# Kernel optimization log

Measured on AMD Instinct MI355X. Metric: run time of the kernel, lower is better.

Reference implementation:

```python
import jax, jax.numpy as jnp
import numpy as np

D_MODEL, EXPAND, D_STATE, D_CONV, HEADDIM = 1024, 2, 64, 4, 64
D_INNER = EXPAND * D_MODEL          # 2048
NHEADS = D_INNER // HEADDIM         # 32
CONV_DIM = D_INNER + 2 * D_STATE    # x, B, C go through the depthwise conv
D_IN_PROJ = 2 * D_INNER + 2 * D_STATE + NHEADS  # z, xBC, dt
EPS = 1e-5


def setup_inputs() -> dict:
    key = jax.random.key(0)
    ks = jax.random.split(key, 16)
    s = 0.02
    inp = {
        "x": jax.random.normal(ks[0], (2, 2048, D_MODEL), jnp.float32),
        "ln1_w": jnp.ones((D_MODEL,), jnp.float32),
        "ln1_b": jnp.zeros((D_MODEL,), jnp.float32),
        "in_proj_w": jax.random.normal(ks[1], (D_IN_PROJ, D_MODEL), jnp.float32) * s,
        "conv_w": jax.random.normal(ks[2], (CONV_DIM, D_CONV), jnp.float32) * 0.3,
        "conv_b": jnp.zeros((CONV_DIM,), jnp.float32),
        # dt_bias so that softplus(dt+dt_bias) lands in ~[1e-3, 0.1] (mamba2 init)
        "dt_bias": jnp.log(jnp.expm1(jnp.exp(jax.random.uniform(ks[3], (NHEADS,), jnp.float32, jnp.log(1e-3), jnp.log(0.1))))),
        "A_log": jnp.log(jax.random.uniform(ks[4], (NHEADS,), jnp.float32, 1.0, 16.0)),
        "D": jnp.ones((NHEADS,), jnp.float32),
        "norm_w": jnp.ones((D_INNER,), jnp.float32),
        "out_proj_w": jax.random.normal(ks[5], (D_MODEL, D_INNER), jnp.float32) * s,
        "ln2_w": jnp.ones((D_MODEL,), jnp.float32),
        "ln2_b": jnp.zeros((D_MODEL,), jnp.float32),
        "mlp_w1": jax.random.normal(ks[6], (4 * D_MODEL, D_MODEL), jnp.float32) * s,
        "mlp_b1": jnp.zeros((4 * D_MODEL,), jnp.float32),
        "mlp_w2": jax.random.normal(ks[7], (D_MODEL, 4 * D_MODEL), jnp.float32) * s,
        "mlp_b2": jnp.zeros((D_MODEL,), jnp.float32),
    }
    return inp


def _layernorm(x, w, b):
    mu = jnp.mean(x, axis=-1, keepdims=True)
    var = jnp.mean(jnp.square(x - mu), axis=-1, keepdims=True)
    return (x - mu) * jax.lax.rsqrt(var + EPS) * w + b


def _mamba2(x, in_proj_w, conv_w, conv_b, dt_bias, A_log, D, norm_w, out_proj_w):
    Bt, L, _ = x.shape
    zxbcdt = x @ in_proj_w.T                                  # [B,L,D_IN_PROJ]
    z = zxbcdt[..., :D_INNER]
    xBC = zxbcdt[..., D_INNER:D_INNER + CONV_DIM]
    dt = jax.nn.softplus(zxbcdt[..., D_INNER + CONV_DIM:] + dt_bias)  # [B,L,H]
    # causal depthwise conv1d, kernel D_CONV, then SiLU
    xp = jnp.pad(xBC, ((0, 0), (D_CONV - 1, 0), (0, 0)))
    conv = conv_b
    for k in range(D_CONV):
        conv = conv + xp[:, k:k + L, :] * conv_w[:, k]
    xBC = jax.nn.silu(conv)
    xs = xBC[..., :D_INNER].reshape(Bt, L, NHEADS, HEADDIM)   # [B,L,H,P]
    Bm = xBC[..., D_INNER:D_INNER + D_STATE]                  # [B,L,N] (ngroups=1)
    Cm = xBC[..., D_INNER + D_STATE:]                         # [B,L,N]
    A = -jnp.exp(A_log)                                       # [H]

    def step(h, inp):
        x_t, dt_t, B_t, C_t = inp                             # [B,H,P],[B,H],[B,N],[B,N]
        dA = jnp.exp(dt_t * A)                                # [B,H]
        h = h * dA[:, :, None, None] + (dt_t[:, :, None] * x_t)[..., None] * B_t[:, None, None, :]
        y = jnp.einsum('bhpn,bn->bhp', h, C_t)
        return h, y

    h0 = jnp.zeros((Bt, NHEADS, HEADDIM, D_STATE), x.dtype)
    xsT = jnp.moveaxis(xs, 1, 0)
    dtT = jnp.moveaxis(dt, 1, 0)
    BT = jnp.moveaxis(Bm, 1, 0)
    CT = jnp.moveaxis(Cm, 1, 0)
    _, ys = jax.lax.scan(step, h0, (xsT, dtT, BT, CT))        # ys: [L,B,H,P]
    y = jnp.moveaxis(ys, 0, 1) + xs * D[None, None, :, None]  # skip D
    y = y.reshape(Bt, L, D_INNER)
    # gated RMSNorm: rmsnorm(y * silu(z)) * norm_w
    y = y * jax.nn.silu(z)
    y = y * jax.lax.rsqrt(jnp.mean(jnp.square(y), axis=-1, keepdims=True) + EPS) * norm_w
    return y @ out_proj_w.T


def reference(x, ln1_w, ln1_b, in_proj_w, conv_w, conv_b, dt_bias, A_log, D,
              norm_w, out_proj_w, ln2_w, ln2_b, mlp_w1, mlp_b1, mlp_w2, mlp_b2):
    res = x
    h = _layernorm(x, ln1_w, ln1_b)
    h = _mamba2(h, in_proj_w, conv_w, conv_b, dt_bias, A_log, D, norm_w, out_proj_w)
    x = res + h
    res = x
    h = _layernorm(x, ln2_w, ln2_b)
    h = jax.nn.gelu(h @ mlp_w1.T + mlp_b1, approximate=False) @ mlp_w2.T + mlp_b2
    return res + h
```

## Files before the change

kernel.cpp:

```cpp
#include <hip/hip_runtime.h>
#include <hip/hip_bf16.h>
#include <math.h>

using bf16 = __hip_bfloat16;
typedef __attribute__((ext_vector_type(8))) short short8;
typedef __attribute__((ext_vector_type(4))) float floatx4;

#define SEQLEN   2048
#define ROWS     4096
#define DMODEL   1024
#define DINNER   2048
#define NHEADS   32
#define HEADDIM  64
#define DSTATE   64
#define CONVDIM  2176
#define DINPROJ  4256
#define NCHUNK   32

__device__ __forceinline__ float b2f(bf16 x) { return __bfloat162float(x); }
__device__ __forceinline__ bf16  f2b(float x) { return __float2bfloat16(x); }
__device__ __forceinline__ float s2f(short s) { union { short s; bf16 b; } u; u.s = s; return b2f(u.b); }
__device__ __forceinline__ short f2s(float f) { union { short s; bf16 b; } u; u.b = f2b(f); return u.s; }
__device__ __forceinline__ float tof(float x) { return x; }
__device__ __forceinline__ float tof(bf16 x)  { return __bfloat162float(x); }

typedef __attribute__((address_space(1))) void v_as1;
typedef __attribute__((address_space(3))) void v_as3;
__device__ __forceinline__ void gload_lds16(const void* g, void* l) {
  __builtin_amdgcn_global_load_lds((v_as1*)(g), (v_as3*)(l), 16, 0, 0);
}

__global__ void cvt_kernel(const float* __restrict__ in, bf16* __restrict__ out, int n4) {
  int i = blockIdx.x * 256 + threadIdx.x;
  if (i < n4) {
    float4 v = ((const float4*)in)[i];
    union { bf16 h[4]; uint2 u; } r;
    r.h[0] = f2b(v.x); r.h[1] = f2b(v.y); r.h[2] = f2b(v.z); r.h[3] = f2b(v.w);
    ((uint2*)out)[i] = r.u;
  }
}

__device__ __forceinline__ void block_reduce_2(float& a, float& b) {
#pragma unroll
  for (int off = 32; off > 0; off >>= 1) {
    a += __shfl_xor(a, off);
    b += __shfl_xor(b, off);
  }
  __shared__ float ra[4], rb[4];
  int w = threadIdx.x >> 6;
  if ((threadIdx.x & 63) == 0) { ra[w] = a; rb[w] = b; }
  __syncthreads();
  a = ra[0] + ra[1] + ra[2] + ra[3];
  b = rb[0] + rb[1] + rb[2] + rb[3];
}

template<typename TIN>
__global__ void ln_kernel(const TIN* __restrict__ x, const float* __restrict__ w,
                          const float* __restrict__ b, bf16* __restrict__ out)
{
  int row = blockIdx.x;
  int tid = threadIdx.x;
  float v[4]; float s = 0.f, sq = 0.f;
#pragma unroll
  for (int k = 0; k < 4; ++k) {
    int c = k * 256 + tid;
    float xv = tof(x[(size_t)row * DMODEL + c]);
    v[k] = xv; s += xv; sq += xv * xv;
  }
  block_reduce_2(s, sq);
  float mu  = s * (1.f / DMODEL);
  float var = sq * (1.f / DMODEL) - mu * mu;
  float rs  = rsqrtf(var + 1e-5f);
#pragma unroll
  for (int k = 0; k < 4; ++k) {
    int c = k * 256 + tid;
    out[(size_t)row * DMODEL + c] = f2b((v[k] - mu) * rs * w[c] + b[c]);
  }
}

template<int EPI>
__device__ __forceinline__ void epi_store(float v, size_t off, int col,
                                          const float* bias, const void* resid, void* Cout)
{
  if (EPI == 0) {
    ((bf16*)Cout)[off] = f2b(v);
  } else if (EPI == 1) {
    v += bias[col];
    v = 0.5f * v * (1.f + erff(v * 0.70710678118654752f));
    ((bf16*)Cout)[off] = f2b(v);
  } else if (EPI == 2) {
    v += ((const float*)resid)[off];
    ((bf16*)Cout)[off] = f2b(v);
  } else {
    v += bias[col] + b2f(((const bf16*)resid)[off]);
    ((float*)Cout)[off] = v;
  }
}


template<int EPI>
__global__ __launch_bounds__(256, 2)
void gemm_bt(const bf16* __restrict__ A, const bf16* __restrict__ W,
             const float* __restrict__ bias, const void* __restrict__ resid,
             void* __restrict__ Cout, int M, int N, int K)
{
  __shared__ __align__(16) short Asl[128 * 64];
  __shared__ __align__(16) short Bsl[128 * 64];
  const int tid  = threadIdx.x;
  const int lane = tid & 63;
  const int wv   = tid >> 6;
  const int wm   = wv >> 1, wn = wv & 1;
  const int r16  = lane & 15, q = lane >> 4;
  const int m0   = blockIdx.x * 128;
  const int n0   = blockIdx.y * 128;

  floatx4 acc[4][4] = {};

  for (int k0 = 0; k0 < K; k0 += 64) {
#pragma unroll
    for (int it = 0; it < 4; ++it) {
      int idx = it * 256 + tid;
      int row = m0 + (idx >> 3);
      int cb  = (((idx & 7) ^ ((idx >> 3) & 7)) << 3);
      gload_lds16(A + (size_t)row * K + k0 + cb, &Asl[idx * 8]);
    }
#pragma unroll
    for (int it = 0; it < 4; ++it) {
      int idx = it * 256 + tid;
      int row = n0 + (idx >> 3);
      if (row > N - 1) row = N - 1;
      int cb  = (((idx & 7) ^ ((idx >> 3) & 7)) << 3);
      gload_lds16(W + (size_t)row * K + k0 + cb, &Bsl[idx * 8]);
    }
    __syncthreads();
#pragma unroll
    for (int kk = 0; kk < 64; kk += 32) {
      short8 af[4], bfr[4];
      const int lb = (kk >> 3) + q;
#pragma unroll
      for (int i = 0; i < 4; ++i) {
        int ar = wm * 64 + i * 16 + r16;
        af[i] = *(const short8*)&Asl[ar * 64 + ((lb ^ (ar & 7)) << 3)];
      }
#pragma unroll
      for (int j = 0; j < 4; ++j) {
        int br = wn * 64 + j * 16 + r16;
        bfr[j] = *(const short8*)&Bsl[br * 64 + ((lb ^ (br & 7)) << 3)];
      }
#pragma unroll
      for (int i = 0; i < 4; ++i)
#pragma unroll
        for (int j = 0; j < 4; ++j)
          acc[i][j] = __builtin_amdgcn_mfma_f32_16x16x32_bf16(af[i], bfr[j], acc[i][j], 0, 0, 0);
    }
    __syncthreads();
  }

#pragma unroll
  for (int i = 0; i < 4; ++i)
#pragma unroll
    for (int j = 0; j < 4; ++j)
#pragma unroll
      for (int r = 0; r < 4; ++r) {
        int row = m0 + wm * 64 + i * 16 + q * 4 + r;
        int col = n0 + wn * 64 + j * 16 + r16;
        if (col < N)
          epi_store<EPI>(acc[i][j][r], (size_t)row * N + col, col, bias, resid, Cout);
      }
}

template<int EPI>
__global__ __launch_bounds__(256, 4)
void gemm_bt_6464(const bf16* __restrict__ A, const bf16* __restrict__ W,
                  const float* __restrict__ bias, const void* __restrict__ resid,
                  void* __restrict__ Cout, int M, int N, int K)
{
  __shared__ __align__(16) short Asl[64 * 64];
  __shared__ __align__(16) short Bsl[64 * 64];
  const int tid  = threadIdx.x;
  const int lane = tid & 63;
  const int wv   = tid >> 6;
  const int wm   = wv >> 1, wn = wv & 1;
  const int r16  = lane & 15, q = lane >> 4;
  const int m0   = blockIdx.x * 64;
  const int n0   = blockIdx.y * 64;

  floatx4 acc[2][2] = {};

  for (int k0 = 0; k0 < K; k0 += 64) {
#pragma unroll
    for (int it = 0; it < 2; ++it) {
      int idx = it * 256 + tid;
      int cb  = (((idx & 7) ^ ((idx >> 3) & 7)) << 3);
      gload_lds16(A + (size_t)(m0 + (idx >> 3)) * K + k0 + cb, &Asl[idx * 8]);
    }
#pragma unroll
    for (int it = 0; it < 2; ++it) {
      int idx = it * 256 + tid;
      int cb  = (((idx & 7) ^ ((idx >> 3) & 7)) << 3);
      gload_lds16(W + (size_t)(n0 + (idx >> 3)) * K + k0 + cb, &Bsl[idx * 8]);
    }
    __syncthreads();
#pragma unroll
    for (int kk = 0; kk < 64; kk += 32) {
      short8 af[2], bfr[2];
      const int lb = (kk >> 3) + q;
#pragma unroll
      for (int i = 0; i < 2; ++i) {
        int ar = wm * 32 + i * 16 + r16;
        af[i] = *(const short8*)&Asl[ar * 64 + ((lb ^ (ar & 7)) << 3)];
      }
#pragma unroll
      for (int j = 0; j < 2; ++j) {
        int br = wn * 32 + j * 16 + r16;
        bfr[j] = *(const short8*)&Bsl[br * 64 + ((lb ^ (br & 7)) << 3)];
      }
#pragma unroll
      for (int i = 0; i < 2; ++i)
#pragma unroll
        for (int j = 0; j < 2; ++j)
          acc[i][j] = __builtin_amdgcn_mfma_f32_16x16x32_bf16(af[i], bfr[j], acc[i][j], 0, 0, 0);
    }
    __syncthreads();
  }

#pragma unroll
  for (int i = 0; i < 2; ++i)
#pragma unroll
    for (int j = 0; j < 2; ++j)
#pragma unroll
      for (int r = 0; r < 4; ++r) {
        int row = m0 + wm * 32 + i * 16 + q * 4 + r;
        int col = n0 + wn * 32 + j * 16 + r16;
        epi_store<EPI>(acc[i][j][r], (size_t)row * N + col, col, bias, resid, Cout);
      }
}

__global__ void conv_kernel(const bf16* __restrict__ zx, const float* __restrict__ cw,
                            const float* __restrict__ cb, const float* __restrict__ dtbias,
                            bf16* __restrict__ xbc, bf16* __restrict__ Bb,
                            bf16* __restrict__ Cbb, float* __restrict__ dtb)
{
  int row = blockIdx.x;
  int b = row >> 11, t = row & 2047;
  for (int c = threadIdx.x; c < CONVDIM; c += 256) {
    float acc = cb[c];
#pragma unroll
    for (int k = 0; k < 4; ++k) {
      int tt = t + k - 3;
      if (tt >= 0)
        acc += b2f(zx[((size_t)(b * SEQLEN + tt)) * DINPROJ + DINNER + c]) * cw[c * 4 + k];
    }
    float s = acc / (1.f + __expf(-acc));
    xbc[(size_t)row * CONVDIM + c] = f2b(s);
    if (c >= DINNER) {
      if (c < DINNER + DSTATE) Bb[row * DSTATE + (c - DINNER)] = f2b(s);
      else                     Cbb[row * DSTATE + (c - DINNER - DSTATE)] = f2b(s);
    }
  }
  if (threadIdx.x < NHEADS) {
    int hh = threadIdx.x;
    float raw = b2f(zx[(size_t)row * DINPROJ + DINNER + CONVDIM + hh]) + dtbias[hh];
    float dt = raw > 20.f ? raw : log1pf(__expf(raw));
    dtb[row * NHEADS + hh] = dt;
  }
}

__device__ __forceinline__ float wave_incl_prefix(float a, int lane) {
#pragma unroll
  for (int off = 1; off < 64; off <<= 1) {
    float o = __shfl_up(a, off);
    if (lane >= off) a += o;
  }
  return a;
}

__global__ __launch_bounds__(64)
void chunk_state_kernel(const bf16* __restrict__ xbc, const bf16* __restrict__ Bb,
                        const float* __restrict__ dtb, const float* __restrict__ A_log,
                        float* __restrict__ Sbuf, float* __restrict__ Pbuf)
{
  const int blk = blockIdx.x;
  const int c = blk & 31, h = (blk >> 5) & 31, b = blk >> 10;
  const int bh = b * 32 + h;
  const int lane = threadIdx.x;
  const int row = b * SEQLEN + c * 64 + lane;
  const float Ah = -__expf(A_log[h]);

  float dts = dtb[row * NHEADS + h];
  float E = wave_incl_prefix(dts * Ah, lane);
  float EQ = __shfl(E, 63);
  float w = __expf(EQ - E) * dts;
  if (lane == 63) Pbuf[bh * NCHUNK + c] = __expf(EQ);

  __shared__ __align__(16) short XwT[64 * 72];
  __shared__ __align__(16) short BT[64 * 72];

  const bf16* xrow = xbc + (size_t)row * CONVDIM + h * 64;
  const bf16* brow = Bb + (size_t)row * DSTATE;
#pragma unroll
  for (int i = 0; i < 8; ++i) {
    short8 xv = *(const short8*)(xrow + i * 8);
    short8 bv = *(const short8*)(brow + i * 8);
#pragma unroll
    for (int j = 0; j < 8; ++j) {
      XwT[(i * 8 + j) * 72 + lane] = f2s(w * s2f(xv[j]));
      BT[(i * 8 + j) * 72 + lane]  = bv[j];
    }
  }
  __syncthreads();

  const int r16 = lane & 15, q = lane >> 4;
  floatx4 acc[4][4] = {};
#pragma unroll
  for (int kk = 0; kk < 64; kk += 32) {
    short8 af[4], bfr[4];
#pragma unroll
    for (int i = 0; i < 4; ++i) af[i]  = *(const short8*)&XwT[(i * 16 + r16) * 72 + kk + q * 8];
#pragma unroll
    for (int j = 0; j < 4; ++j) bfr[j] = *(const short8*)&BT[(j * 16 + r16) * 72 + kk + q * 8];
#pragma unroll
    for (int i = 0; i < 4; ++i)
#pragma unroll
      for (int j = 0; j < 4; ++j)
        acc[i][j] = __builtin_amdgcn_mfma_f32_16x16x32_bf16(af[i], bfr[j], acc[i][j], 0, 0, 0);
  }
  float* Sout = Sbuf + (size_t)(bh * NCHUNK + c) * 4096;
#pragma unroll
  for (int i = 0; i < 4; ++i)
#pragma unroll
    for (int j = 0; j < 4; ++j)
#pragma unroll
      for (int r = 0; r < 4; ++r)
        Sout[(i * 16 + q * 4 + r) * 64 + (j * 16 + r16)] = acc[i][j][r];
}

__global__ __launch_bounds__(64)
void combine_kernel(const float* __restrict__ Sbuf, const float* __restrict__ Pbuf,
                    bf16* __restrict__ HinB)
{
  const int bh = blockIdx.x >> 2, slab = blockIdx.x & 3;
  const int base = slab * 1024 + threadIdx.x * 16;
  float h[16];
#pragma unroll
  for (int k = 0; k < 16; ++k) h[k] = 0.f;
  for (int c = 0; c < NCHUNK; ++c) {
    size_t off = (size_t)(bh * NCHUNK + c) * 4096 + base;
    union { short s[16]; uint4 q[2]; } pk;
#pragma unroll
    for (int k = 0; k < 16; ++k) pk.s[k] = f2s(h[k]);
    *(uint4*)(HinB + off)     = pk.q[0];
    *(uint4*)(HinB + off + 8) = pk.q[1];
    float P = Pbuf[bh * NCHUNK + c];
    const float4* S4 = (const float4*)(Sbuf + off);
#pragma unroll
    for (int k = 0; k < 4; ++k) {
      float4 s = S4[k];
      h[k*4+0] = h[k*4+0] * P + s.x;
      h[k*4+1] = h[k*4+1] * P + s.y;
      h[k*4+2] = h[k*4+2] * P + s.z;
      h[k*4+3] = h[k*4+3] * P + s.w;
    }
  }
}

__global__ __launch_bounds__(64)
void y_kernel(const bf16* __restrict__ xbc, const bf16* __restrict__ Bb,
              const bf16* __restrict__ Cbb, const float* __restrict__ dtb,
              const bf16* __restrict__ HinB, const float* __restrict__ A_log,
              const float* __restrict__ Dp, bf16* __restrict__ yout)
{
  const int blk = blockIdx.x;
  const int c = blk & 31, h = (blk >> 5) & 31, b = blk >> 10;
  const int bh = b * 32 + h;
  const int lane = threadIdx.x;
  const int row0 = b * SEQLEN + c * 64;
  const int row = row0 + lane;
  const float Ah = -__expf(A_log[h]);
  const float Dh = Dp[h];

  __shared__ __align__(16) short XdT[64 * 72];
  __shared__ __align__(16) short Msh[64 * 72];
  __shared__ float Esh[64];

  float dts = dtb[row * NHEADS + h];
  float E = wave_incl_prefix(dts * Ah, lane);
  Esh[lane] = E;

  const bf16* xrow = xbc + (size_t)row * CONVDIM + h * 64;
#pragma unroll
  for (int i = 0; i < 8; ++i) {
    short8 xv = *(const short8*)(xrow + i * 8);
#pragma unroll
    for (int j = 0; j < 8; ++j)
      XdT[(i * 8 + j) * 72 + lane] = f2s(dts * s2f(xv[j]));
  }
  __syncthreads();

  const int r16 = lane & 15, q = lane >> 4;

  floatx4 accg[4][4] = {};
#pragma unroll
  for (int kk = 0; kk < 64; kk += 32) {
    short8 af[4], bfr[4];
#pragma unroll
    for (int i = 0; i < 4; ++i)
      af[i]  = *(const short8*)(Cbb + (size_t)(row0 + i * 16 + r16) * DSTATE + kk + q * 8);
#pragma unroll
    for (int j = 0; j < 4; ++j)
      bfr[j] = *(const short8*)(Bb + (size_t)(row0 + j * 16 + r16) * DSTATE + kk + q * 8);
#pragma unroll
    for (int i = 0; i < 4; ++i)
#pragma unroll
      for (int j = 0; j < 4; ++j)
        accg[i][j] = __builtin_amdgcn_mfma_f32_16x16x32_bf16(af[i], bfr[j], accg[i][j], 0, 0, 0);
  }
#pragma unroll
  for (int i = 0; i < 4; ++i)
#pragma unroll
    for (int j = 0; j < 4; ++j)
#pragma unroll
      for (int r = 0; r < 4; ++r) {
        int t = i * 16 + q * 4 + r;
        int s = j * 16 + r16;
        float v = (s <= t) ? __expf(Esh[t] - Esh[s]) * accg[i][j][r] : 0.f;
        Msh[t * 72 + s] = f2s(v);
      }
  __syncthreads();

  floatx4 acc[4][4] = {};
#pragma unroll
  for (int kk = 0; kk < 64; kk += 32) {
    short8 af[4], bfr[4];
#pragma unroll
    for (int i = 0; i < 4; ++i) af[i]  = *(const short8*)&Msh[(i * 16 + r16) * 72 + kk + q * 8];
#pragma unroll
    for (int j = 0; j < 4; ++j) bfr[j] = *(const short8*)&XdT[(j * 16 + r16) * 72 + kk + q * 8];
#pragma unroll
    for (int i = 0; i < 4; ++i)
#pragma unroll
      for (int j = 0; j < 4; ++j)
        acc[i][j] = __builtin_amdgcn_mfma_f32_16x16x32_bf16(af[i], bfr[j], acc[i][j], 0, 0, 0);
  }
  float ei[4];
#pragma unroll
  for (int i = 0; i < 4; ++i) ei[i] = __expf(Esh[i * 16 + r16]);
  const bf16* hinp = HinB + (size_t)(bh * NCHUNK + c) * 4096;
#pragma unroll
  for (int kk = 0; kk < 64; kk += 32) {
    short8 af[4], bfr[4];
#pragma unroll
    for (int i = 0; i < 4; ++i) {
      short8 cv = *(const short8*)(Cbb + (size_t)(row0 + i * 16 + r16) * DSTATE + kk + q * 8);
#pragma unroll
      for (int jj = 0; jj < 8; ++jj) af[i][jj] = f2s(ei[i] * s2f(cv[jj]));
    }
#pragma unroll
    for (int j = 0; j < 4; ++j)
      bfr[j] = *(const short8*)(hinp + (j * 16 + r16) * 64 + kk + q * 8);
#pragma unroll
    for (int i = 0; i < 4; ++i)
#pragma unroll
      for (int j = 0; j < 4; ++j)
        acc[i][j] = __builtin_amdgcn_mfma_f32_16x16x32_bf16(af[i], bfr[j], acc[i][j], 0, 0, 0);
  }
#pragma unroll
  for (int i = 0; i < 4; ++i)
#pragma unroll
    for (int j = 0; j < 4; ++j)
#pragma unroll
      for (int r = 0; r < 4; ++r) {
        int t = i * 16 + q * 4 + r;
        int p = j * 16 + r16;
        int g = row0 + t;
        float y = acc[i][j][r] + Dh * b2f(xbc[(size_t)g * CONVDIM + h * 64 + p]);
        yout[(size_t)g * DINNER + h * 64 + p] = f2b(y);
      }
}

__global__ void gate_rms_kernel(const bf16* __restrict__ y, const bf16* __restrict__ zx,
                                const float* __restrict__ nw, bf16* __restrict__ yn)
{
  int row = blockIdx.x, tid = threadIdx.x;
  float v[8]; float ss = 0.f, dummy = 0.f;
#pragma unroll
  for (int k = 0; k < 8; ++k) {
    int c = k * 256 + tid;
    float z = b2f(zx[(size_t)row * DINPROJ + c]);
    float g = z / (1.f + __expf(-z));
    float val = b2f(y[(size_t)row * DINNER + c]) * g;
    v[k] = val; ss += val * val;
  }
  block_reduce_2(ss, dummy);
  float rs = rsqrtf(ss * (1.f / DINNER) + 1e-5f);
#pragma unroll
  for (int k = 0; k < 8; ++k) {
    int c = k * 256 + tid;
    yn[(size_t)row * DINNER + c] = f2b(v[k] * rs * nw[c]);
  }
}

extern "C" void kernel_launch(void* const* d_in, const int* in_sizes, int n_in,
                              void* d_out, int out_size, void* d_ws, size_t ws_size,
                              hipStream_t stream)
{
  const float* x         = (const float*)d_in[0];
  const float* ln1_w     = (const float*)d_in[1];
  const float* ln1_b     = (const float*)d_in[2];
  const float* in_proj_w = (const float*)d_in[3];
  const float* conv_w    = (const float*)d_in[4];
  const float* conv_b    = (const float*)d_in[5];
  const float* dt_bias   = (const float*)d_in[6];
  const float* A_log     = (const float*)d_in[7];
  const float* Dp        = (const float*)d_in[8];
  const float* norm_w    = (const float*)d_in[9];
  const float* out_proj_w= (const float*)d_in[10];
  const float* ln2_w     = (const float*)d_in[11];
  const float* ln2_b     = (const float*)d_in[12];
  const float* mlp_w1    = (const float*)d_in[13];
  const float* mlp_b1    = (const float*)d_in[14];
  const float* mlp_w2    = (const float*)d_in[15];
  const float* mlp_b2    = (const float*)d_in[16];

  char* ws = (char*)d_ws;
  bf16*  zx   = (bf16*)(ws + 0);
  bf16*  h1   = (bf16*)(ws + 34865152);
  bf16*  xbc  = (bf16*)(ws + 43253760);
  bf16*  Bb   = (bf16*)(ws + 61079552);
  bf16*  Cbb  = (bf16*)(ws + 61603840);
  float* dtb  = (float*)(ws + 62128128);
  float* Pbuf = (float*)(ws + 62652416);
  float* Sbuf = (float*)(ws + 62660608);
  bf16*  yw   = (bf16*)(ws + 62660608);
  bf16*  x2   = (bf16*)(ws + 79437824);
  bf16*  HinB = (bf16*)(ws + 96215040);
  bf16*  yn   = (bf16*)(ws + 96215040);
  bf16*  wip  = (bf16*)(ws + 112992256);
  bf16*  wop  = (bf16*)(ws + 121708544);
  bf16*  h2n  = h1;
  bf16*  mid  = zx;
  bf16*  w1b  = wip;
  bf16*  w2b  = xbc;

  cvt_kernel<<<(4256 * 1024 / 4 + 255) / 256, 256, 0, stream>>>(in_proj_w, wip, 4256 * 1024 / 4);
  ln_kernel<float><<<ROWS, 256, 0, stream>>>(x, ln1_w, ln1_b, h1);
  gemm_bt<0><<<dim3(32, 34), 256, 0, stream>>>(h1, wip, nullptr, nullptr, zx,
                                               ROWS, DINPROJ, DMODEL);
  cvt_kernel<<<(4096 * 1024 / 4 + 255) / 256, 256, 0, stream>>>(mlp_w1, w1b, 4096 * 1024 / 4);
  cvt_kernel<<<(1024 * 2048 / 4 + 255) / 256, 256, 0, stream>>>(out_proj_w, wop, 1024 * 2048 / 4);
  conv_kernel<<<ROWS, 256, 0, stream>>>(zx, conv_w, conv_b, dt_bias, xbc, Bb, Cbb, dtb);
  chunk_state_kernel<<<2048, 64, 0, stream>>>(xbc, Bb, dtb, A_log, Sbuf, Pbuf);
  combine_kernel<<<256, 64, 0, stream>>>(Sbuf, Pbuf, HinB);
  y_kernel<<<2048, 64, 0, stream>>>(xbc, Bb, Cbb, dtb, HinB, A_log, Dp, yw);
  cvt_kernel<<<(1024 * 4096 / 4 + 255) / 256, 256, 0, stream>>>(mlp_w2, w2b, 1024 * 4096 / 4);
  gate_rms_kernel<<<ROWS, 256, 0, stream>>>(yw, zx, norm_w, yn);
  gemm_bt_6464<2><<<dim3(64, 16), 256, 0, stream>>>(yn, wop, nullptr, x, (void*)x2,
                                                    ROWS, DMODEL, DINNER);
  ln_kernel<bf16><<<ROWS, 256, 0, stream>>>(x2, ln2_w, ln2_b, h2n);
  gemm_bt<1><<<dim3(32, 32), 256, 0, stream>>>(h2n, w1b, mlp_b1, nullptr, mid,
                                               ROWS, 4 * DMODEL, DMODEL);
  gemm_bt_6464<3><<<dim3(64, 16), 256, 0, stream>>>(mid, w2b, mlp_b2, x2, d_out,
                                                    ROWS, DMODEL, 4 * DMODEL);
}
```

Baseline: 427.4 us.

## Double-buffer GEMM LDS tiles with 32-wide K steps and prefetch

Both bf16 MFMA GEMM kernels now keep two LDS buffers of 32-wide K tiles and issue the async global-to-LDS loads for the next tile before computing on the current one. This needs one barrier per step instead of two. The aim is to hide global load latency behind MFMA work. The trade-off is that each K step does half as much compute per barrier, and the new 4-block XOR swizzle may change LDS bank-conflict behaviour.

New measurement: 443.6 us. 3.8% more time.

```diff
diff --git a/kernel.cpp b/kernel.cpp
--- a/kernel.cpp
+++ b/kernel.cpp
@@ -29,6 +29,8 @@
 __device__ __forceinline__ void gload_lds16(const void* g, void* l) {
   __builtin_amdgcn_global_load_lds((v_as1*)(g), (v_as3*)(l), 16, 0, 0);
 }
+
+__device__ __forceinline__ int swz(int row) { return (row & 3) ^ ((row >> 1) & 2); }
 
 __global__ void cvt_kernel(const float* __restrict__ in, bf16* __restrict__ out, int n4) {
   int i = blockIdx.x * 256 + threadIdx.x;
@@ -97,15 +99,14 @@
   }
 }
 
-
 template<int EPI>
 __global__ __launch_bounds__(256, 2)
 void gemm_bt(const bf16* __restrict__ A, const bf16* __restrict__ W,
              const float* __restrict__ bias, const void* __restrict__ resid,
              void* __restrict__ Cout, int M, int N, int K)
 {
-  __shared__ __align__(16) short Asl[128 * 64];
-  __shared__ __align__(16) short Bsl[128 * 64];
+  __shared__ __align__(16) short Asl[2][128 * 32];
+  __shared__ __align__(16) short Bsl[2][128 * 32];
   const int tid  = threadIdx.x;
   const int lane = tid & 63;
   const int wv   = tid >> 6;
@@ -113,47 +114,49 @@
   const int r16  = lane & 15, q = lane >> 4;
   const int m0   = blockIdx.x * 128;
   const int n0   = blockIdx.y * 128;
+  const int nk   = K >> 5;
 
   floatx4 acc[4][4] = {};
 
-  for (int k0 = 0; k0 < K; k0 += 64) {
-#pragma unroll
-    for (int it = 0; it < 4; ++it) {
+  auto stage = [&](int buf, int k0) {
+#pragma unroll
+    for (int it = 0; it < 2; ++it) {
       int idx = it * 256 + tid;
-      int row = m0 + (idx >> 3);
-      int cb  = (((idx & 7) ^ ((idx >> 3) & 7)) << 3);
-      gload_lds16(A + (size_t)row * K + k0 + cb, &Asl[idx * 8]);
-    }
-#pragma unroll
-    for (int it = 0; it < 4; ++it) {
+      int row = idx >> 2, pos = idx & 3;
+      int sb  = pos ^ swz(row);
+      gload_lds16(A + (size_t)(m0 + row) * K + k0 + sb * 8, &Asl[buf][idx * 8]);
+    }
+#pragma unroll
+    for (int it = 0; it < 2; ++it) {
       int idx = it * 256 + tid;
-      int row = n0 + (idx >> 3);
-      if (row > N - 1) row = N - 1;
-      int cb  = (((idx & 7) ^ ((idx >> 3) & 7)) << 3);
-      gload_lds16(W + (size_t)row * K + k0 + cb, &Bsl[idx * 8]);
-    }
+      int row = idx >> 2, pos = idx & 3;
+      int grow = n0 + row; if (grow > N - 1) grow = N - 1;
+      int sb  = pos ^ swz(row);
+      gload_lds16(W + (size_t)grow * K + k0 + sb * 8, &Bsl[buf][idx * 8]);
+    }
+  };
+
+  stage(0, 0);
+  for (int k = 0; k < nk; ++k) {
     __syncthreads();
-#pragma unroll
-    for (int kk = 0; kk < 64; kk += 32) {
-      short8 af[4], bfr[4];
-      const int lb = (kk >> 3) + q;
-#pragma unroll
-      for (int i = 0; i < 4; ++i) {
-        int ar = wm * 64 + i * 16 + r16;
-        af[i] = *(const short8*)&Asl[ar * 64 + ((lb ^ (ar & 7)) << 3)];
-      }
-#pragma unroll
-      for (int j = 0; j < 4; ++j) {
-        int br = wn * 64 + j * 16 + r16;
-        bfr[j] = *(const short8*)&Bsl[br * 64 + ((lb ^ (br & 7)) << 3)];
-      }
-#pragma unroll
-      for (int i = 0; i < 4; ++i)
-#pragma unroll
-        for (int j = 0; j < 4; ++j)
-          acc[i][j] = __builtin_amdgcn_mfma_f32_16x16x32_bf16(af[i], bfr[j], acc[i][j], 0, 0, 0);
-    }
-    __syncthreads();
+    if (k + 1 < nk) stage((k + 1) & 1, (k + 1) << 5);
+    const int cur = k & 1;
+    short8 af[4], bfr[4];
+#pragma unroll
+    for (int i = 0; i < 4; ++i) {
+      int ar = wm * 64 + i * 16 + r16;
+      af[i] = *(const short8*)&Asl[cur][ar * 32 + ((q ^ swz(ar)) << 3)];
+    }
+#pragma unroll
+    for (int j = 0; j < 4; ++j) {
+      int br = wn * 64 + j * 16 + r16;
+      bfr[j] = *(const short8*)&Bsl[cur][br * 32 + ((q ^ swz(br)) << 3)];
+    }
+#pragma unroll
+    for (int i = 0; i < 4; ++i)
+#pragma unroll
+      for (int j = 0; j < 4; ++j)
+        acc[i][j] = __builtin_amdgcn_mfma_f32_16x16x32_bf16(af[i], bfr[j], acc[i][j], 0, 0, 0);
   }
 
 #pragma unroll
@@ -175,8 +178,8 @@
                   const float* __restrict__ bias, const void* __restrict__ resid,
                   void* __restrict__ Cout, int M, int N, int K)
 {
-  __shared__ __align__(16) short Asl[64 * 64];
-  __shared__ __align__(16) short Bsl[64 * 64];
+  __shared__ __align__(16) short Asl[2][64 * 32];
+  __shared__ __align__(16) short Bsl[2][64 * 32];
   const int tid  = threadIdx.x;
   const int lane = tid & 63;
   const int wv   = tid >> 6;
@@ -184,44 +187,44 @@
   const int r16  = lane & 15, q = lane >> 4;
   const int m0   = blockIdx.x * 64;
   const int n0   = blockIdx.y * 64;
+  const int nk   = K >> 5;
 
   floatx4 acc[2][2] = {};
 
-  for (int k0 = 0; k0 < K; k0 += 64) {
-#pragma unroll
-    for (int it = 0; it < 2; ++it) {
-      int idx = it * 256 + tid;
-      int cb  = (((idx & 7) ^ ((idx >> 3) & 7)) << 3);
-      gload_lds16(A + (size_t)(m0 + (idx >> 3)) * K + k0 + cb, &Asl[idx * 8]);
-    }
-#pragma unroll
-    for (int it = 0; it < 2; ++it) {
-      int idx = it * 256 + tid;
-      int cb  = (((idx & 7) ^ ((idx >> 3) & 7)) << 3);
-      gload_lds16(W + (size_t)(n0 + (idx >> 3)) * K + k0 + cb, &Bsl[idx * 8]);
-    }
+  auto stage = [&](int buf, int k0) {
+    {
+      int row = tid >> 2, pos = tid & 3;
+      int sb  = pos ^ swz(row);
+      gload_lds16(A + (size_t)(m0 + row) * K + k0 + sb * 8, &Asl[buf][tid * 8]);
+    }
+    {
+      int row = tid >> 2, pos = tid & 3;
+      int sb  = pos ^ swz(row);
+      gload_lds16(W + (size_t)(n0 + row) * K + k0 + sb * 8, &Bsl[buf][tid * 8]);
+    }
+  };
+
+  stage(0, 0);
+  for (int k = 0; k < nk; ++k) {
     __syncthreads();
-#pragma unroll
-    for (int kk = 0; kk < 64; kk += 32) {
-      short8 af[2], bfr[2];
-      const int lb = (kk >> 3) + q;
-#pragma unroll
-      for (int i = 0; i < 2; ++i) {
-        int ar = wm * 32 + i * 16 + r16;
-        af[i] = *(const short8*)&Asl[ar * 64 + ((lb ^ (ar & 7)) << 3)];
-      }
-#pragma unroll
-      for (int j = 0; j < 2; ++j) {
-        int br = wn * 32 + j * 16 + r16;
-        bfr[j] = *(const short8*)&Bsl[br * 64 + ((lb ^ (br & 7)) << 3)];
-      }
-#pragma unroll
-      for (int i = 0; i < 2; ++i)
-#pragma unroll
-        for (int j = 0; j < 2; ++j)
-          acc[i][j] = __builtin_amdgcn_mfma_f32_16x16x32_bf16(af[i], bfr[j], acc[i][j], 0, 0, 0);
-    }
-    __syncthreads();
+    if (k + 1 < nk) stage((k + 1) & 1, (k + 1) << 5);
+    const int cur = k & 1;
+    short8 af[2], bfr[2];
+#pragma unroll
+    for (int i = 0; i < 2; ++i) {
+      int ar = wm * 32 + i * 16 + r16;
+      af[i] = *(const short8*)&Asl[cur][ar * 32 + ((q ^ swz(ar)) << 3)];
+    }
+#pragma unroll
+    for (int j = 0; j < 2; ++j) {
+      int br = wn * 32 + j * 16 + r16;
+      bfr[j] = *(const short8*)&Bsl[cur][br * 32 + ((q ^ swz(br)) << 3)];
+    }
+#pragma unroll
+    for (int i = 0; i < 2; ++i)
+#pragma unroll
+      for (int j = 0; j < 2; ++j)
+        acc[i][j] = __builtin_amdgcn_mfma_f32_16x16x32_bf16(af[i], bfr[j], acc[i][j], 0, 0, 0);
   }
 
 #pragma unroll
```
